# Optimization experiments

Hardware: AMD Instinct MI355X
Metric: run time of the kernel (lower is better)

Reference implementation:

```python
import jax, jax.numpy as jnp
import numpy as np

N, E, D_IN, D_HID, D_OUT = 50000, 800000, 128, 128, 300
BN_EPS = 1e-5


def setup_inputs() -> dict:
    key = jax.random.key(0)
    ks = jax.random.split(key, 10)
    s_in = 1.0 / np.sqrt(D_IN)
    s_hid = 1.0 / np.sqrt(D_HID)
    return {
        "x": jax.random.normal(ks[0], (N, D_IN), jnp.float32),
        "edge_index": jax.random.randint(ks[1], (2, E), 0, N, jnp.int64),
        "Wl": jax.random.normal(ks[2], (D_IN, D_HID), jnp.float32) * s_in,
        "bl": jnp.zeros((D_HID,), jnp.float32),
        "Wr": jax.random.normal(ks[3], (D_IN, D_HID), jnp.float32) * s_in,
        "Wsk": jax.random.normal(ks[4], (D_IN, D_HID), jnp.float32) * s_in,
        "bsk": jnp.zeros((D_HID,), jnp.float32),
        "gamma": jnp.ones((D_HID,), jnp.float32),
        "beta": jnp.zeros((D_HID,), jnp.float32),
        "rmean": jnp.zeros((D_HID,), jnp.float32),
        "rvar": jnp.ones((D_HID,), jnp.float32),
        "Wlo": jax.random.normal(ks[5], (D_HID, D_OUT), jnp.float32) * s_hid,
        "blo": jnp.zeros((D_OUT,), jnp.float32),
        "Wro": jax.random.normal(ks[6], (D_HID, D_OUT), jnp.float32) * s_hid,
    }


def sage_conv(x, src, dst, n_nodes, W_l, b_l, W_r):
    # PyG SAGEConv (aggr='mean'): lin_l(mean_{j in N(i)} x_j) + lin_r(x_i)
    msgs = x[src]                                                 # [E, d] gather
    agg = jax.ops.segment_sum(msgs, dst, num_segments=n_nodes)    # [N, d]
    cnt = jax.ops.segment_sum(jnp.ones((src.shape[0], 1), x.dtype), dst,
                              num_segments=n_nodes)               # [N, 1]
    mean = agg / jnp.maximum(cnt, 1.0)
    return mean @ W_l + b_l + x @ W_r


def reference(x, edge_index, Wl, bl, Wr, Wsk, bsk, gamma, beta, rmean, rvar,
              Wlo, blo, Wro):
    src, dst = edge_index[0], edge_index[1]
    n = x.shape[0]
    # layer 0: conv + skip linear
    h = sage_conv(x, src, dst, n, Wl, bl, Wr) + (x @ Wsk + bsk)
    # BatchNorm1d (eval: running stats)
    h = (h - rmean) * (gamma * jax.lax.rsqrt(rvar + BN_EPS)) + beta
    x_emb = jax.nn.relu(h)                                        # dropout: no-op in eval
    # output conv + log_softmax
    x_out = sage_conv(x_emb, src, dst, n, Wlo, blo, Wro)
    return h, jax.nn.log_softmax(x_out, axis=1)
```

## Files before the change

kernel.cpp:

```cpp
#include <hip/hip_runtime.h>

typedef __attribute__((__ext_vector_type__(8))) __bf16 bf16x8;
typedef __attribute__((__ext_vector_type__(4))) float f32x4;
typedef __attribute__((__ext_vector_type__(4))) unsigned int u32x4;

__device__ __forceinline__ float bf2f(unsigned short u) {
    return __uint_as_float(((unsigned int)u) << 16);
}
__device__ __forceinline__ unsigned short f2bf(float f) {
    unsigned int u = __float_as_uint(f);
    u += 0x7FFFu + ((u >> 16) & 1u);
    return (unsigned short)(u >> 16);
}

__device__ __forceinline__ bool low_short_is_bf16like(unsigned int w) {
    unsigned int lo = w & 0xFFFFu;
    if (lo == 0u || lo == 0x8000u) return true;
    unsigned int e = (lo >> 7) & 0xFFu;
    return (e >= 0x6Cu && e <= 0x8Cu);
}

__global__ __launch_bounds__(64) void k_detect(
    const unsigned int* __restrict__ x, const unsigned int* __restrict__ wl,
    const unsigned int* __restrict__ ei, int* __restrict__ flags)
{
    int t = threadIdx.x;
    int xv = __popcll(__ballot(low_short_is_bf16like(x[t])));
    int wv = __popcll(__ballot(low_short_is_bf16like(wl[t])));
    unsigned int o1 = ei[2 * t + 1];
    unsigned int o2 = ei[2 * t + 129];
    bool oddzero = (o1 == 0u) && (o2 == 0u);
    int e64 = __all(oddzero) ? 1 : 0;
    if (t == 0) {
        flags[0] = (xv < 32) ? 1 : 0;
        flags[1] = (wv < 32) ? 1 : 0;
        flags[2] = e64;
    }
}

__global__ __launch_bounds__(256) void k_tobf(
    const void* __restrict__ xv, const int* __restrict__ flags,
    unsigned short* __restrict__ xbf, long nelem)
{
    int xf32 = flags[0];
    long i = ((long)blockIdx.x * 256 + threadIdx.x) * 8;
    if (i >= nelem) return;
    if (xf32) {
        const float4* p = (const float4*)((const float*)xv + i);
        float4 v0 = p[0], v1 = p[1];
        u32x4 o;
        o.x = (unsigned int)f2bf(v0.x) | ((unsigned int)f2bf(v0.y) << 16);
        o.y = (unsigned int)f2bf(v0.z) | ((unsigned int)f2bf(v0.w) << 16);
        o.z = (unsigned int)f2bf(v1.x) | ((unsigned int)f2bf(v1.y) << 16);
        o.w = (unsigned int)f2bf(v1.z) | ((unsigned int)f2bf(v1.w) << 16);
        *(u32x4*)&xbf[i] = o;
    } else {
        *(u32x4*)&xbf[i] = *(const u32x4*)((const unsigned short*)xv + i);
    }
}

__global__ __launch_bounds__(256) void k_fold1(
    const void* __restrict__ Wl, const void* __restrict__ Wr,
    const void* __restrict__ Wsk, const void* __restrict__ gamma,
    const void* __restrict__ rvar, const int* __restrict__ flags,
    unsigned short* __restrict__ W1p)
{
    int wf32 = flags[1];
    int idx = blockIdx.x * 256 + threadIdx.x;
    int kb = idx >> 10;
    int c  = (idx >> 3) & 127;
    int k7 = idx & 7;
    int k  = kb * 8 + k7;
    float g, rv, w;
    if (wf32) {
        g  = ((const float*)gamma)[c];
        rv = ((const float*)rvar)[c];
        if (k < 128) w = ((const float*)Wl)[k * 128 + c];
        else { int kk = k - 128;
               w = ((const float*)Wr)[kk * 128 + c] + ((const float*)Wsk)[kk * 128 + c]; }
    } else {
        g  = bf2f(((const unsigned short*)gamma)[c]);
        rv = bf2f(((const unsigned short*)rvar)[c]);
        if (k < 128) w = bf2f(((const unsigned short*)Wl)[k * 128 + c]);
        else { int kk = k - 128;
               w = bf2f(((const unsigned short*)Wr)[kk * 128 + c]) +
                   bf2f(((const unsigned short*)Wsk)[kk * 128 + c]); }
    }
    float s = g * rsqrtf(rv + 1e-5f);
    W1p[idx] = f2bf(w * s);
}

__global__ __launch_bounds__(256) void k_fold2(
    const void* __restrict__ Wlo, const void* __restrict__ Wro,
    const int* __restrict__ flags, unsigned short* __restrict__ W2p)
{
    int wf32 = flags[1];
    int idx = blockIdx.x * 256 + threadIdx.x;
    int kb  = idx / 2560;
    int rem = idx - kb * 2560;
    int c   = rem >> 3;
    int k7  = idx & 7;
    int k   = kb * 8 + k7;
    float w = 0.f;
    if (c < 300) {
        if (wf32)
            w = (k < 128) ? ((const float*)Wlo)[k * 300 + c]
                          : ((const float*)Wro)[(k - 128) * 300 + c];
        else
            w = (k < 128) ? bf2f(((const unsigned short*)Wlo)[k * 300 + c])
                          : bf2f(((const unsigned short*)Wro)[(k - 128) * 300 + c]);
    }
    W2p[idx] = f2bf(w);
}

__global__ __launch_bounds__(512) void k_foldb(
    const void* __restrict__ bl, const void* __restrict__ bsk,
    const void* __restrict__ rmean, const void* __restrict__ beta,
    const void* __restrict__ gamma, const void* __restrict__ rvar,
    const void* __restrict__ blo, const int* __restrict__ flags,
    float* __restrict__ bias1, float* __restrict__ bias2)
{
    int wf32 = flags[1];
    int t = threadIdx.x;
    if (t < 128) {
        float g, rv, b1, b2, rm, be;
        if (wf32) {
            g = ((const float*)gamma)[t]; rv = ((const float*)rvar)[t];
            b1 = ((const float*)bl)[t];   b2 = ((const float*)bsk)[t];
            rm = ((const float*)rmean)[t]; be = ((const float*)beta)[t];
        } else {
            g = bf2f(((const unsigned short*)gamma)[t]); rv = bf2f(((const unsigned short*)rvar)[t]);
            b1 = bf2f(((const unsigned short*)bl)[t]);   b2 = bf2f(((const unsigned short*)bsk)[t]);
            rm = bf2f(((const unsigned short*)rmean)[t]); be = bf2f(((const unsigned short*)beta)[t]);
        }
        float s = g * rsqrtf(rv + 1e-5f);
        bias1[t] = (b1 + b2 - rm) * s + be;
    } else if (t < 448) {
        int c = t - 128;
        float b = 0.f;
        if (c < 300)
            b = wf32 ? ((const float*)blo)[c] : bf2f(((const unsigned short*)blo)[c]);
        bias2[c] = b;
    }
}

__global__ __launch_bounds__(256) void k_rank(
    const int* __restrict__ ei, const int* __restrict__ flags,
    int* __restrict__ deg, int* __restrict__ rank, int E, int nnodes)
{
    int e64 = flags[2];
    int e = blockIdx.x * 256 + threadIdx.x;
    if (e >= E) return;
    int d = e64 ? ei[2 * (E + e)] : ei[E + e];
    int r = 0;
    if ((unsigned)d < (unsigned)nnodes) r = atomicAdd(&deg[d], 1);
    rank[e] = r;
}

template <typename IT>
__global__ __launch_bounds__(256) void k_place(
    const int* __restrict__ ei, const int* __restrict__ flags,
    const int* __restrict__ rowptr, const int* __restrict__ aux,
    const int* __restrict__ rank,
    IT* __restrict__ adj, int E, int nnodes)
{
    int e64 = flags[2];
    int e = blockIdx.x * 256 + threadIdx.x;
    if (e >= E) return;
    int s, d;
    if (e64) { s = ei[2 * e]; d = ei[2 * (E + e)]; }
    else     { s = ei[e];     d = ei[E + e]; }
    if ((unsigned)d >= (unsigned)nnodes) return;
    if ((unsigned)s >= (unsigned)nnodes) s = 0;
    adj[rowptr[d] + aux[d >> 10] + rank[e]] = (IT)s;
}

__global__ __launch_bounds__(256) void k_scan_a(
    const int* __restrict__ deg, int* __restrict__ rowptr,
    int* __restrict__ aux, int n)
{
    __shared__ int wsum[4];
    int t = threadIdx.x, blk = blockIdx.x;
    int base = blk * 1024 + t * 4;
    int v[4];
    int s = 0;
    #pragma unroll
    for (int i = 0; i < 4; i++) { int idx = base + i; v[i] = (idx < n) ? deg[idx] : 0; s += v[i]; }
    int lane = t & 63, wv = t >> 6;
    int inc = s;
    #pragma unroll
    for (int off = 1; off < 64; off <<= 1) {
        int u = __shfl_up(inc, off);
        if (lane >= off) inc += u;
    }
    if (lane == 63) wsum[wv] = inc;
    __syncthreads();
    int woff = 0;
    if (wv >= 1) woff += wsum[0];
    if (wv >= 2) woff += wsum[1];
    if (wv >= 3) woff += wsum[2];
    int exc = woff + inc - s;
    #pragma unroll
    for (int i = 0; i < 4; i++) { int idx = base + i; if (idx < n) rowptr[idx] = exc; exc += v[i]; }
    if (t == 255) aux[blk] = woff + inc;
}

__global__ __launch_bounds__(64) void k_scan_b(int* __restrict__ aux, int nblk)
{
    int t = threadIdx.x;
    int carry = 0;
    for (int base = 0; base < nblk; base += 64) {
        int idx = base + t;
        int v = (idx < nblk) ? aux[idx] : 0;
        int inc = v;
        #pragma unroll
        for (int off = 1; off < 64; off <<= 1) {
            int u = __shfl_up(inc, off);
            if (t >= off) inc += u;
        }
        if (idx < nblk) aux[idx] = carry + inc - v;
        carry += __shfl(inc, 63);
    }
}

template <typename IT>
__global__ __launch_bounds__(256) void k_agg(
    const unsigned short* __restrict__ xB,
    const int* __restrict__ rowptr, const int* __restrict__ aux,
    const int* __restrict__ deg,
    const IT* __restrict__ adj, unsigned short* __restrict__ meanB, int n)
{
    int wid = (blockIdx.x * 256 + threadIdx.x) >> 6;
    if (wid >= n) return;
    int lane = threadIdx.x & 63;
    int h  = lane >> 5;
    int sl = lane & 31;
    int start = rowptr[wid] + aux[wid >> 10];
    int dc = deg[wid];
    float acc[4][4];
    #pragma unroll
    for (int u = 0; u < 4; u++)
        #pragma unroll
        for (int c = 0; c < 4; c++) acc[u][c] = 0.f;
    int i = 0;
    for (; i + 7 < dc; i += 8) {
        int e0 = (int)adj[start + i + h];
        int e1 = (int)adj[start + i + 2 + h];
        int e2 = (int)adj[start + i + 4 + h];
        int e3 = (int)adj[start + i + 6 + h];
        uint2 p0 = *(const uint2*)&xB[(size_t)e0 * 128 + sl * 4];
        uint2 p1 = *(const uint2*)&xB[(size_t)e1 * 128 + sl * 4];
        uint2 p2 = *(const uint2*)&xB[(size_t)e2 * 128 + sl * 4];
        uint2 p3 = *(const uint2*)&xB[(size_t)e3 * 128 + sl * 4];
        acc[0][0] += bf2f((unsigned short)p0.x); acc[0][1] += bf2f((unsigned short)(p0.x >> 16));
        acc[0][2] += bf2f((unsigned short)p0.y); acc[0][3] += bf2f((unsigned short)(p0.y >> 16));
        acc[1][0] += bf2f((unsigned short)p1.x); acc[1][1] += bf2f((unsigned short)(p1.x >> 16));
        acc[1][2] += bf2f((unsigned short)p1.y); acc[1][3] += bf2f((unsigned short)(p1.y >> 16));
        acc[2][0] += bf2f((unsigned short)p2.x); acc[2][1] += bf2f((unsigned short)(p2.x >> 16));
        acc[2][2] += bf2f((unsigned short)p2.y); acc[2][3] += bf2f((unsigned short)(p2.y >> 16));
        acc[3][0] += bf2f((unsigned short)p3.x); acc[3][1] += bf2f((unsigned short)(p3.x >> 16));
        acc[3][2] += bf2f((unsigned short)p3.y); acc[3][3] += bf2f((unsigned short)(p3.y >> 16));
    }
    for (; i + h < dc; i += 2) {
        int e0 = (int)adj[start + i + h];
        uint2 p0 = *(const uint2*)&xB[(size_t)e0 * 128 + sl * 4];
        acc[0][0] += bf2f((unsigned short)p0.x); acc[0][1] += bf2f((unsigned short)(p0.x >> 16));
        acc[0][2] += bf2f((unsigned short)p0.y); acc[0][3] += bf2f((unsigned short)(p0.y >> 16));
    }
    float t0 = (acc[0][0] + acc[1][0]) + (acc[2][0] + acc[3][0]);
    float t1 = (acc[0][1] + acc[1][1]) + (acc[2][1] + acc[3][1]);
    float t2 = (acc[0][2] + acc[1][2]) + (acc[2][2] + acc[3][2]);
    float t3 = (acc[0][3] + acc[1][3]) + (acc[2][3] + acc[3][3]);
    t0 += __shfl_xor(t0, 32);
    t1 += __shfl_xor(t1, 32);
    t2 += __shfl_xor(t2, 32);
    t3 += __shfl_xor(t3, 32);
    if (h == 0) {
        float inv = 1.f / fmaxf((float)dc, 1.f);
        uint2 o;
        o.x = (unsigned int)f2bf(t0 * inv) | ((unsigned int)f2bf(t1 * inv) << 16);
        o.y = (unsigned int)f2bf(t2 * inv) | ((unsigned int)f2bf(t3 * inv) << 16);
        *(uint2*)&meanB[(size_t)wid * 128 + sl * 4] = o;
    }
}

__global__ __launch_bounds__(256) void k_gemm1(
    const unsigned short* __restrict__ meanB,
    const unsigned short* __restrict__ xbf, const int* __restrict__ flags,
    const unsigned short* __restrict__ Wp,
    const float* __restrict__ bias, void* __restrict__ outh,
    unsigned short* __restrict__ xemb, int nrows)
{
    constexpr int NTW = 2;
    __shared__ __align__(16) unsigned short Alds[32 * 264];
    int tid = threadIdx.x;
    int row0 = blockIdx.x * 32;
    int xf32 = flags[0];
    {
        int r = tid >> 3, c0 = (tid & 7) * 16;
        int rg = row0 + r; if (rg >= nrows) rg = nrows - 1;
        const u32x4* mp = (const u32x4*)(meanB + (size_t)rg * 128 + c0);
        *(u32x4*)&Alds[r * 264 + c0]     = mp[0];
        *(u32x4*)&Alds[r * 264 + c0 + 8] = mp[1];
        const u32x4* xp = (const u32x4*)(xbf + (size_t)rg * 128 + c0);
        *(u32x4*)&Alds[r * 264 + 128 + c0]     = xp[0];
        *(u32x4*)&Alds[r * 264 + 128 + c0 + 8] = xp[1];
    }
    __syncthreads();
    f32x4 acc[2][NTW];
    #pragma unroll
    for (int a = 0; a < 2; a++)
        #pragma unroll
        for (int b = 0; b < NTW; b++) acc[a][b] = f32x4{0.f, 0.f, 0.f, 0.f};
    int lane = tid & 63, wv = tid >> 6, lh = lane & 15, lq = lane >> 4;
    #pragma unroll
    for (int ks = 0; ks < 8; ++ks) {
        bf16x8 a0 = *(const bf16x8*)&Alds[lh * 264 + ks * 32 + lq * 8];
        bf16x8 a1 = *(const bf16x8*)&Alds[(16 + lh) * 264 + ks * 32 + lq * 8];
        #pragma unroll
        for (int i = 0; i < NTW; i++) {
            int col = (wv + 4 * i) * 16 + lh;
            bf16x8 bfr = *(const bf16x8*)&Wp[(ks * 4 + lq) * 1024 + col * 8];
            acc[0][i] = __builtin_amdgcn_mfma_f32_16x16x32_bf16(a0, bfr, acc[0][i], 0, 0, 0);
            acc[1][i] = __builtin_amdgcn_mfma_f32_16x16x32_bf16(a1, bfr, acc[1][i], 0, 0, 0);
        }
    }
    float* outF = (float*)outh;
    unsigned short* outB = (unsigned short*)outh;
    #pragma unroll
    for (int rt = 0; rt < 2; ++rt)
        #pragma unroll
        for (int i = 0; i < NTW; i++)
            #pragma unroll
            for (int j = 0; j < 4; j++) {
                int r = row0 + rt * 16 + lq * 4 + j;
                if (r < nrows) {
                    int c = (wv + 4 * i) * 16 + lh;
                    float v = acc[rt][i][j] + bias[c];
                    if (xf32) outF[(size_t)r * 128 + c] = v;
                    else      outB[(size_t)r * 128 + c] = f2bf(v);
                    xemb[(size_t)r * 128 + c] = f2bf(fmaxf(v, 0.f));
                }
            }
}

__global__ __launch_bounds__(256) void k_gemm2(
    const unsigned short* __restrict__ meanB,
    const unsigned short* __restrict__ xf, const unsigned short* __restrict__ Wp,
    const float* __restrict__ bias, const int* __restrict__ flags,
    void* __restrict__ outbase, int nrows)
{
    constexpr int NTW = 5;
    __shared__ __align__(16) unsigned short Alds[32 * 264];
    __shared__ float redM[4][32];
    __shared__ float redS[4][32];
    int tid = threadIdx.x;
    int row0 = blockIdx.x * 32;
    int xf32 = flags[0];
    {
        int r = tid >> 3, c0 = (tid & 7) * 16;
        int rg = row0 + r; if (rg >= nrows) rg = nrows - 1;
        const u32x4* mp = (const u32x4*)(meanB + (size_t)rg * 128 + c0);
        *(u32x4*)&Alds[r * 264 + c0]     = mp[0];
        *(u32x4*)&Alds[r * 264 + c0 + 8] = mp[1];
        const u32x4* xp = (const u32x4*)(xf + (size_t)rg * 128 + c0);
        *(u32x4*)&Alds[r * 264 + 128 + c0]     = xp[0];
        *(u32x4*)&Alds[r * 264 + 128 + c0 + 8] = xp[1];
    }
    __syncthreads();
    f32x4 acc[2][NTW];
    #pragma unroll
    for (int a = 0; a < 2; a++)
        #pragma unroll
        for (int b = 0; b < NTW; b++) acc[a][b] = f32x4{0.f, 0.f, 0.f, 0.f};
    int lane = tid & 63, wv = tid >> 6, lh = lane & 15, lq = lane >> 4;
    #pragma unroll
    for (int ks = 0; ks < 8; ++ks) {
        bf16x8 a0 = *(const bf16x8*)&Alds[lh * 264 + ks * 32 + lq * 8];
        bf16x8 a1 = *(const bf16x8*)&Alds[(16 + lh) * 264 + ks * 32 + lq * 8];
        #pragma unroll
        for (int i = 0; i < NTW; i++) {
            int col = (wv + 4 * i) * 16 + lh;
            bf16x8 bfr = *(const bf16x8*)&Wp[(ks * 4 + lq) * 2560 + col * 8];
            acc[0][i] = __builtin_amdgcn_mfma_f32_16x16x32_bf16(a0, bfr, acc[0][i], 0, 0, 0);
            acc[1][i] = __builtin_amdgcn_mfma_f32_16x16x32_bf16(a1, bfr, acc[1][i], 0, 0, 0);
        }
    }
    #pragma unroll
    for (int rt = 0; rt < 2; ++rt)
        #pragma unroll
        for (int i = 0; i < NTW; i++) {
            int col = (wv + 4 * i) * 16 + lh;
            float b = bias[col];
            #pragma unroll
            for (int j = 0; j < 4; j++) acc[rt][i][j] += b;
        }
    float M[2][4];
    #pragma unroll
    for (int rt = 0; rt < 2; ++rt)
        #pragma unroll
        for (int j = 0; j < 4; j++) {
            float m = -3.0e38f;
            #pragma unroll
            for (int i = 0; i < NTW; i++) {
                int col = (wv + 4 * i) * 16 + lh;
                if (col < 300) m = fmaxf(m, acc[rt][i][j]);
            }
            m = fmaxf(m, __shfl_xor(m, 1, 16));
            m = fmaxf(m, __shfl_xor(m, 2, 16));
            m = fmaxf(m, __shfl_xor(m, 4, 16));
            m = fmaxf(m, __shfl_xor(m, 8, 16));
            M[rt][j] = m;
        }
    if (lh == 0) {
        #pragma unroll
        for (int rt = 0; rt < 2; ++rt)
            #pragma unroll
            for (int j = 0; j < 4; j++)
                redM[wv][rt * 16 + lq * 4 + j] = M[rt][j];
    }
    __syncthreads();
    #pragma unroll
    for (int rt = 0; rt < 2; ++rt)
        #pragma unroll
        for (int j = 0; j < 4; j++) {
            int rl = rt * 16 + lq * 4 + j;
            M[rt][j] = fmaxf(fmaxf(redM[0][rl], redM[1][rl]),
                             fmaxf(redM[2][rl], redM[3][rl]));
        }
    float S[2][4];
    #pragma unroll
    for (int rt = 0; rt < 2; ++rt)
        #pragma unroll
        for (int j = 0; j < 4; j++) {
            float s = 0.f;
            #pragma unroll
            for (int i = 0; i < NTW; i++) {
                int col = (wv + 4 * i) * 16 + lh;
                if (col < 300) s += __expf(acc[rt][i][j] - M[rt][j]);
            }
            s += __shfl_xor(s, 1, 16);
            s += __shfl_xor(s, 2, 16);
            s += __shfl_xor(s, 4, 16);
            s += __shfl_xor(s, 8, 16);
            S[rt][j] = s;
        }
    if (lh == 0) {
        #pragma unroll
        for (int rt = 0; rt < 2; ++rt)
            #pragma unroll
            for (int j = 0; j < 4; j++)
                redS[wv][rt * 16 + lq * 4 + j] = S[rt][j];
    }
    __syncthreads();
    float* out1F = (float*)outbase + (size_t)nrows * 128;
    unsigned short* out1B = (unsigned short*)outbase + (size_t)nrows * 128;
    #pragma unroll
    for (int rt = 0; rt < 2; ++rt)
        #pragma unroll
        for (int j = 0; j < 4; j++) {
            int rl = rt * 16 + lq * 4 + j;
            float Sall = (redS[0][rl] + redS[1][rl]) + (redS[2][rl] + redS[3][rl]);
            float L = M[rt][j] + __logf(Sall);
            int rg = row0 + rl;
            if (rg < nrows) {
                #pragma unroll
                for (int i = 0; i < NTW; i++) {
                    int col = (wv + 4 * i) * 16 + lh;
                    if (col < 300) {
                        float v = acc[rt][i][j] - L;
                        if (xf32) out1F[(size_t)rg * 300 + col] = v;
                        else      out1B[(size_t)rg * 300 + col] = f2bf(v);
                    }
                }
            }
        }
}

extern "C" void kernel_launch(void* const* d_in, const int* in_sizes, int n_in,
                              void* d_out, int out_size, void* d_ws, size_t ws_size,
                              hipStream_t stream)
{
    const void* x     = d_in[0];
    const int*  ei    = (const int*)d_in[1];
    const void* Wl    = d_in[2];
    const void* bl    = d_in[3];
    const void* Wr    = d_in[4];
    const void* Wsk   = d_in[5];
    const void* bsk   = d_in[6];
    const void* gamma = d_in[7];
    const void* beta  = d_in[8];
    const void* rmean = d_in[9];
    const void* rvar  = d_in[10];
    const void* Wlo   = d_in[11];
    const void* blo   = d_in[12];
    const void* Wro   = d_in[13];

    int N = in_sizes[0] / 128;
    int E = in_sizes[1] / 2;
    long nelem = (long)N * 128;
    bool idx16 = (N <= 65535);

    char* ws = (char*)d_ws;
    size_t off = 0;
    int* flags = (int*)(ws + off);            off += 256;
    unsigned short* xbf   = (unsigned short*)(ws + off); off += (size_t)N * 128 * 2;
    unsigned short* meanB = (unsigned short*)(ws + off); off += (size_t)N * 128 * 2;
    unsigned short* xemb  = (unsigned short*)(ws + off); off += (size_t)N * 128 * 2;
    off = (off + 255) & ~(size_t)255;
    int* deg    = (int*)(ws + off);           off += (size_t)N * 4;
    int* rowptr = (int*)(ws + off);           off += (size_t)N * 4;
    int* rank   = (int*)(ws + off);           off += (size_t)E * 4;
    int* aux    = (int*)(ws + off);           off += 256;
    void* adjv  = (void*)(ws + off);          off += (size_t)E * 4;
    off = (off + 255) & ~(size_t)255;
    unsigned short* W1p = (unsigned short*)(ws + off);  off += 32768 * 2;
    unsigned short* W2p = (unsigned short*)(ws + off);  off += 81920 * 2;
    float* bias1 = (float*)(ws + off);        off += 512;
    float* bias2 = (float*)(ws + off);        off += 1280;

    int egrid = (E + 255) / 256;
    int sblk  = (N + 1023) / 1024;
    int agrid = (N + 3) / 4;
    int ggrid = (N + 31) / 32;
    int tgrid = (int)((nelem / 8 + 255) / 256);

    hipMemsetAsync(deg, 0, (size_t)N * 4, stream);
    k_detect<<<1, 64, 0, stream>>>((const unsigned int*)x, (const unsigned int*)Wl,
                                   (const unsigned int*)ei, flags);
    k_tobf<<<tgrid, 256, 0, stream>>>(x, flags, xbf, nelem);
    k_fold1<<<128, 256, 0, stream>>>(Wl, Wr, Wsk, gamma, rvar, flags, W1p);
    k_fold2<<<320, 256, 0, stream>>>(Wlo, Wro, flags, W2p);
    k_foldb<<<1, 512, 0, stream>>>(bl, bsk, rmean, beta, gamma, rvar, blo, flags, bias1, bias2);

    k_rank<<<egrid, 256, 0, stream>>>(ei, flags, deg, rank, E, N);
    k_scan_a<<<sblk, 256, 0, stream>>>(deg, rowptr, aux, N);
    k_scan_b<<<1, 64, 0, stream>>>(aux, sblk);

    if (idx16) {
        unsigned short* adj = (unsigned short*)adjv;
        k_place<unsigned short><<<egrid, 256, 0, stream>>>(ei, flags, rowptr, aux, rank, adj, E, N);
        k_agg<unsigned short><<<agrid, 256, 0, stream>>>(xbf, rowptr, aux, deg, adj, meanB, N);
        k_gemm1<<<ggrid, 256, 0, stream>>>(meanB, xbf, flags, W1p, bias1, d_out, xemb, N);
        k_agg<unsigned short><<<agrid, 256, 0, stream>>>(xemb, rowptr, aux, deg, adj, meanB, N);
        k_gemm2<<<ggrid, 256, 0, stream>>>(meanB, xemb, W2p, bias2, flags, d_out, N);
    } else {
        int* adj = (int*)adjv;
        k_place<int><<<egrid, 256, 0, stream>>>(ei, flags, rowptr, aux, rank, adj, E, N);
        k_agg<int><<<agrid, 256, 0, stream>>>(xbf, rowptr, aux, deg, adj, meanB, N);
        k_gemm1<<<ggrid, 256, 0, stream>>>(meanB, xbf, flags, W1p, bias1, d_out, xemb, N);
        k_agg<int><<<agrid, 256, 0, stream>>>(xemb, rowptr, aux, deg, adj, meanB, N);
        k_gemm2<<<ggrid, 256, 0, stream>>>(meanB, xemb, W2p, bias2, flags, d_out, N);
    }
}
```

Before: 191.0 us.

## Gather neighbor features in fp8 and fuse setup kernels, drop flag detection

Quantizes node features (input x and the layer-1 embedding) to fp8 copies and has the mean-aggregation gather read 1 byte per element instead of 2 bf16 bytes, halving the random-gather traffic. The type-detection kernel is removed in favor of inline probing in each kernel. The deg memset is folded into the conversion kernel and the three weight/bias fold kernels are merged into one launch. An extra conversion pass over xemb is added, and the fp8 quantization of aggregated features lowers accuracy, which may break tolerance.

```diff
diff --git a/kernel.cpp b/kernel.cpp
--- a/kernel.cpp
+++ b/kernel.cpp
@@ -2,6 +2,7 @@
 
 typedef __attribute__((__ext_vector_type__(8))) __bf16 bf16x8;
 typedef __attribute__((__ext_vector_type__(4))) float f32x4;
+typedef __attribute__((__ext_vector_type__(2))) float f32x2;
 typedef __attribute__((__ext_vector_type__(4))) unsigned int u32x4;
 
 __device__ __forceinline__ float bf2f(unsigned short u) {
@@ -19,136 +20,158 @@
     unsigned int e = (lo >> 7) & 0xFFu;
     return (e >= 0x6Cu && e <= 0x8Cu);
 }
-
-__global__ __launch_bounds__(64) void k_detect(
-    const unsigned int* __restrict__ x, const unsigned int* __restrict__ wl,
-    const unsigned int* __restrict__ ei, int* __restrict__ flags)
-{
-    int t = threadIdx.x;
-    int xv = __popcll(__ballot(low_short_is_bf16like(x[t])));
-    int wv = __popcll(__ballot(low_short_is_bf16like(wl[t])));
+__device__ __forceinline__ int probe_f32(const unsigned int* __restrict__ p) {
+    int t = threadIdx.x & 63;
+    int cnt = __popcll(__ballot(low_short_is_bf16like(p[t])));
+    return (cnt < 32) ? 1 : 0;
+}
+__device__ __forceinline__ int probe_e64(const unsigned int* __restrict__ ei) {
+    int t = threadIdx.x & 63;
     unsigned int o1 = ei[2 * t + 1];
     unsigned int o2 = ei[2 * t + 129];
-    bool oddzero = (o1 == 0u) && (o2 == 0u);
-    int e64 = __all(oddzero) ? 1 : 0;
-    if (t == 0) {
-        flags[0] = (xv < 32) ? 1 : 0;
-        flags[1] = (wv < 32) ? 1 : 0;
-        flags[2] = e64;
-    }
+    return __all((o1 == 0u) && (o2 == 0u)) ? 1 : 0;
 }
 
 __global__ __launch_bounds__(256) void k_tobf(
-    const void* __restrict__ xv, const int* __restrict__ flags,
-    unsigned short* __restrict__ xbf, long nelem)
-{
-    int xf32 = flags[0];
+    const void* __restrict__ xv, unsigned short* __restrict__ xbf,
+    unsigned int* __restrict__ x8, int* __restrict__ deg,
+    long nelem, int n, int tgrid)
+{
+    if ((int)blockIdx.x >= tgrid) {
+        int j = ((int)blockIdx.x - tgrid) * 256 + threadIdx.x;
+        if (j < n) deg[j] = 0;
+        return;
+    }
+    int xf32 = probe_f32((const unsigned int*)xv);
     long i = ((long)blockIdx.x * 256 + threadIdx.x) * 8;
     if (i >= nelem) return;
+    float f[8];
     if (xf32) {
         const float4* p = (const float4*)((const float*)xv + i);
         float4 v0 = p[0], v1 = p[1];
+        f[0] = v0.x; f[1] = v0.y; f[2] = v0.z; f[3] = v0.w;
+        f[4] = v1.x; f[5] = v1.y; f[6] = v1.z; f[7] = v1.w;
         u32x4 o;
-        o.x = (unsigned int)f2bf(v0.x) | ((unsigned int)f2bf(v0.y) << 16);
-        o.y = (unsigned int)f2bf(v0.z) | ((unsigned int)f2bf(v0.w) << 16);
-        o.z = (unsigned int)f2bf(v1.x) | ((unsigned int)f2bf(v1.y) << 16);
-        o.w = (unsigned int)f2bf(v1.z) | ((unsigned int)f2bf(v1.w) << 16);
+        o.x = (unsigned int)f2bf(f[0]) | ((unsigned int)f2bf(f[1]) << 16);
+        o.y = (unsigned int)f2bf(f[2]) | ((unsigned int)f2bf(f[3]) << 16);
+        o.z = (unsigned int)f2bf(f[4]) | ((unsigned int)f2bf(f[5]) << 16);
+        o.w = (unsigned int)f2bf(f[6]) | ((unsigned int)f2bf(f[7]) << 16);
         *(u32x4*)&xbf[i] = o;
     } else {
-        *(u32x4*)&xbf[i] = *(const u32x4*)((const unsigned short*)xv + i);
-    }
-}
-
-__global__ __launch_bounds__(256) void k_fold1(
+        u32x4 v = *(const u32x4*)((const unsigned short*)xv + i);
+        *(u32x4*)&xbf[i] = v;
+        f[0] = bf2f((unsigned short)v.x); f[1] = bf2f((unsigned short)(v.x >> 16));
+        f[2] = bf2f((unsigned short)v.y); f[3] = bf2f((unsigned short)(v.y >> 16));
+        f[4] = bf2f((unsigned short)v.z); f[5] = bf2f((unsigned short)(v.z >> 16));
+        f[6] = bf2f((unsigned short)v.w); f[7] = bf2f((unsigned short)(v.w >> 16));
+    }
+    unsigned int q0 = 0, q1 = 0;
+    q0 = (unsigned int)__builtin_amdgcn_cvt_pk_fp8_f32(f[0], f[1], (int)q0, false);
+    q0 = (unsigned int)__builtin_amdgcn_cvt_pk_fp8_f32(f[2], f[3], (int)q0, true);
+    q1 = (unsigned int)__builtin_amdgcn_cvt_pk_fp8_f32(f[4], f[5], (int)q1, false);
+    q1 = (unsigned int)__builtin_amdgcn_cvt_pk_fp8_f32(f[6], f[7], (int)q1, true);
+    uint2 q; q.x = q0; q.y = q1;
+    *(uint2*)&x8[i >> 2] = q;
+}
+
+__global__ __launch_bounds__(256) void k_to8(
+    const unsigned short* __restrict__ src, unsigned int* __restrict__ dst,
+    long nelem)
+{
+    long i = ((long)blockIdx.x * 256 + threadIdx.x) * 8;
+    if (i >= nelem) return;
+    u32x4 v = *(const u32x4*)&src[i];
+    unsigned int q0 = 0, q1 = 0;
+    q0 = (unsigned int)__builtin_amdgcn_cvt_pk_fp8_f32(
+            bf2f((unsigned short)v.x), bf2f((unsigned short)(v.x >> 16)), (int)q0, false);
+    q0 = (unsigned int)__builtin_amdgcn_cvt_pk_fp8_f32(
+            bf2f((unsigned short)v.y), bf2f((unsigned short)(v.y >> 16)), (int)q0, true);
+    q1 = (unsigned int)__builtin_amdgcn_cvt_pk_fp8_f32(
+            bf2f((unsigned short)v.z), bf2f((unsigned short)(v.z >> 16)), (int)q1, false);
+    q1 = (unsigned int)__builtin_amdgcn_cvt_pk_fp8_f32(
+            bf2f((unsigned short)v.w), bf2f((unsigned short)(v.w >> 16)), (int)q1, true);
+    uint2 q; q.x = q0; q.y = q1;
+    *(uint2*)&dst[i >> 2] = q;
+}
+
+__global__ __launch_bounds__(256) void k_fold(
     const void* __restrict__ Wl, const void* __restrict__ Wr,
     const void* __restrict__ Wsk, const void* __restrict__ gamma,
-    const void* __restrict__ rvar, const int* __restrict__ flags,
-    unsigned short* __restrict__ W1p)
-{
-    int wf32 = flags[1];
-    int idx = blockIdx.x * 256 + threadIdx.x;
-    int kb = idx >> 10;
-    int c  = (idx >> 3) & 127;
-    int k7 = idx & 7;
-    int k  = kb * 8 + k7;
-    float g, rv, w;
-    if (wf32) {
-        g  = ((const float*)gamma)[c];
-        rv = ((const float*)rvar)[c];
-        if (k < 128) w = ((const float*)Wl)[k * 128 + c];
-        else { int kk = k - 128;
-               w = ((const float*)Wr)[kk * 128 + c] + ((const float*)Wsk)[kk * 128 + c]; }
+    const void* __restrict__ rvar, const void* __restrict__ bl,
+    const void* __restrict__ bsk, const void* __restrict__ rmean,
+    const void* __restrict__ beta, const void* __restrict__ Wlo,
+    const void* __restrict__ blo, const void* __restrict__ Wro,
+    unsigned short* __restrict__ W1p, unsigned short* __restrict__ W2p,
+    float* __restrict__ bias1, float* __restrict__ bias2)
+{
+    int wf32 = probe_f32((const unsigned int*)Wl);
+    int b = blockIdx.x, t = threadIdx.x;
+    if (b < 128) {
+        int idx = b * 256 + t;
+        int kb = idx >> 10, c = (idx >> 3) & 127, k7 = idx & 7;
+        int k = kb * 8 + k7;
+        float g, rv, w;
+        if (wf32) {
+            g  = ((const float*)gamma)[c];
+            rv = ((const float*)rvar)[c];
+            if (k < 128) w = ((const float*)Wl)[k * 128 + c];
+            else { int kk = k - 128;
+                   w = ((const float*)Wr)[kk * 128 + c] + ((const float*)Wsk)[kk * 128 + c]; }
+        } else {
+            g  = bf2f(((const unsigned short*)gamma)[c]);
+            rv = bf2f(((const unsigned short*)rvar)[c]);
+            if (k < 128) w = bf2f(((const unsigned short*)Wl)[k * 128 + c]);
+            else { int kk = k - 128;
+                   w = bf2f(((const unsigned short*)Wr)[kk * 128 + c]) +
+                       bf2f(((const unsigned short*)Wsk)[kk * 128 + c]); }
+        }
+        float s = g * rsqrtf(rv + 1e-5f);
+        W1p[idx] = f2bf(w * s);
+    } else if (b < 448) {
+        int idx = (b - 128) * 256 + t;
+        int kb = idx / 2560;
+        int rem = idx - kb * 2560;
+        int c = rem >> 3, k7 = idx & 7;
+        int k = kb * 8 + k7;
+        float w = 0.f;
+        if (c < 300) {
+            if (wf32)
+                w = (k < 128) ? ((const float*)Wlo)[k * 300 + c]
+                              : ((const float*)Wro)[(k - 128) * 300 + c];
+            else
+                w = (k < 128) ? bf2f(((const unsigned short*)Wlo)[k * 300 + c])
+                              : bf2f(((const unsigned short*)Wro)[(k - 128) * 300 + c]);
+        }
+        W2p[idx] = f2bf(w);
     } else {
-        g  = bf2f(((const unsigned short*)gamma)[c]);
-        rv = bf2f(((const unsigned short*)rvar)[c]);
-        if (k < 128) w = bf2f(((const unsigned short*)Wl)[k * 128 + c]);
-        else { int kk = k - 128;
-               w = bf2f(((const unsigned short*)Wr)[kk * 128 + c]) +
-                   bf2f(((const unsigned short*)Wsk)[kk * 128 + c]); }
-    }
-    float s = g * rsqrtf(rv + 1e-5f);
-    W1p[idx] = f2bf(w * s);
-}
-
-__global__ __launch_bounds__(256) void k_fold2(
-    const void* __restrict__ Wlo, const void* __restrict__ Wro,
-    const int* __restrict__ flags, unsigned short* __restrict__ W2p)
-{
-    int wf32 = flags[1];
-    int idx = blockIdx.x * 256 + threadIdx.x;
-    int kb  = idx / 2560;
-    int rem = idx - kb * 2560;
-    int c   = rem >> 3;
-    int k7  = idx & 7;
-    int k   = kb * 8 + k7;
-    float w = 0.f;
-    if (c < 300) {
-        if (wf32)
-            w = (k < 128) ? ((const float*)Wlo)[k * 300 + c]
-                          : ((const float*)Wro)[(k - 128) * 300 + c];
-        else
-            w = (k < 128) ? bf2f(((const unsigned short*)Wlo)[k * 300 + c])
-                          : bf2f(((const unsigned short*)Wro)[(k - 128) * 300 + c]);
-    }
-    W2p[idx] = f2bf(w);
-}
-
-__global__ __launch_bounds__(512) void k_foldb(
-    const void* __restrict__ bl, const void* __restrict__ bsk,
-    const void* __restrict__ rmean, const void* __restrict__ beta,
-    const void* __restrict__ gamma, const void* __restrict__ rvar,
-    const void* __restrict__ blo, const int* __restrict__ flags,
-    float* __restrict__ bias1, float* __restrict__ bias2)
-{
-    int wf32 = flags[1];
-    int t = threadIdx.x;
-    if (t < 128) {
-        float g, rv, b1, b2, rm, be;
-        if (wf32) {
-            g = ((const float*)gamma)[t]; rv = ((const float*)rvar)[t];
-            b1 = ((const float*)bl)[t];   b2 = ((const float*)bsk)[t];
-            rm = ((const float*)rmean)[t]; be = ((const float*)beta)[t];
-        } else {
-            g = bf2f(((const unsigned short*)gamma)[t]); rv = bf2f(((const unsigned short*)rvar)[t]);
-            b1 = bf2f(((const unsigned short*)bl)[t]);   b2 = bf2f(((const unsigned short*)bsk)[t]);
-            rm = bf2f(((const unsigned short*)rmean)[t]); be = bf2f(((const unsigned short*)beta)[t]);
-        }
-        float s = g * rsqrtf(rv + 1e-5f);
-        bias1[t] = (b1 + b2 - rm) * s + be;
-    } else if (t < 448) {
-        int c = t - 128;
-        float b = 0.f;
-        if (c < 300)
-            b = wf32 ? ((const float*)blo)[c] : bf2f(((const unsigned short*)blo)[c]);
-        bias2[c] = b;
+        if (t < 128) {
+            float g, rv, b1, b2, rm, be;
+            if (wf32) {
+                g = ((const float*)gamma)[t]; rv = ((const float*)rvar)[t];
+                b1 = ((const float*)bl)[t];   b2 = ((const float*)bsk)[t];
+                rm = ((const float*)rmean)[t]; be = ((const float*)beta)[t];
+            } else {
+                g = bf2f(((const unsigned short*)gamma)[t]); rv = bf2f(((const unsigned short*)rvar)[t]);
+                b1 = bf2f(((const unsigned short*)bl)[t]);   b2 = bf2f(((const unsigned short*)bsk)[t]);
+                rm = bf2f(((const unsigned short*)rmean)[t]); be = bf2f(((const unsigned short*)beta)[t]);
+            }
+            float s = g * rsqrtf(rv + 1e-5f);
+            bias1[t] = (b1 + b2 - rm) * s + be;
+        }
+        for (int c = t; c < 320; c += 256) {
+            float v = 0.f;
+            if (c < 300)
+                v = wf32 ? ((const float*)blo)[c] : bf2f(((const unsigned short*)blo)[c]);
+            bias2[c] = v;
+        }
     }
 }
 
 __global__ __launch_bounds__(256) void k_rank(
-    const int* __restrict__ ei, const int* __restrict__ flags,
+    const int* __restrict__ ei,
     int* __restrict__ deg, int* __restrict__ rank, int E, int nnodes)
 {
-    int e64 = flags[2];
+    int e64 = probe_e64((const unsigned int*)ei);
     int e = blockIdx.x * 256 + threadIdx.x;
     if (e >= E) return;
     int d = e64 ? ei[2 * (E + e)] : ei[E + e];
@@ -159,12 +182,12 @@
 
 template <typename IT>
 __global__ __launch_bounds__(256) void k_place(
-    const int* __restrict__ ei, const int* __restrict__ flags,
+    const int* __restrict__ ei,
     const int* __restrict__ rowptr, const int* __restrict__ aux,
     const int* __restrict__ rank,
     IT* __restrict__ adj, int E, int nnodes)
 {
-    int e64 = flags[2];
+    int e64 = probe_e64((const unsigned int*)ei);
     int e = blockIdx.x * 256 + threadIdx.x;
     if (e >= E) return;
     int s, d;
@@ -225,7 +248,7 @@
 
 template <typename IT>
 __global__ __launch_bounds__(256) void k_agg(
-    const unsigned short* __restrict__ xB,
+    const unsigned int* __restrict__ x8,
     const int* __restrict__ rowptr, const int* __restrict__ aux,
     const int* __restrict__ deg,
     const IT* __restrict__ adj, unsigned short* __restrict__ meanB, int n)
@@ -248,24 +271,29 @@
         int e1 = (int)adj[start + i + 2 + h];
         int e2 = (int)adj[start + i + 4 + h];
         int e3 = (int)adj[start + i + 6 + h];
-        uint2 p0 = *(const uint2*)&xB[(size_t)e0 * 128 + sl * 4];
-        uint2 p1 = *(const uint2*)&xB[(size_t)e1 * 128 + sl * 4];
-        uint2 p2 = *(const uint2*)&xB[(size_t)e2 * 128 + sl * 4];
-        uint2 p3 = *(const uint2*)&xB[(size_t)e3 * 128 + sl * 4];
-        acc[0][0] += bf2f((unsigned short)p0.x); acc[0][1] += bf2f((unsigned short)(p0.x >> 16));
-        acc[0][2] += bf2f((unsigned short)p0.y); acc[0][3] += bf2f((unsigned short)(p0.y >> 16));
-        acc[1][0] += bf2f((unsigned short)p1.x); acc[1][1] += bf2f((unsigned short)(p1.x >> 16));
-        acc[1][2] += bf2f((unsigned short)p1.y); acc[1][3] += bf2f((unsigned short)(p1.y >> 16));
-        acc[2][0] += bf2f((unsigned short)p2.x); acc[2][1] += bf2f((unsigned short)(p2.x >> 16));
-        acc[2][2] += bf2f((unsigned short)p2.y); acc[2][3] += bf2f((unsigned short)(p2.y >> 16));
-        acc[3][0] += bf2f((unsigned short)p3.x); acc[3][1] += bf2f((unsigned short)(p3.x >> 16));
-        acc[3][2] += bf2f((unsigned short)p3.y); acc[3][3] += bf2f((unsigned short)(p3.y >> 16));
+        unsigned int p0 = x8[(size_t)e0 * 32 + sl];
+        unsigned int p1 = x8[(size_t)e1 * 32 + sl];
+        unsigned int p2 = x8[(size_t)e2 * 32 + sl];
+        unsigned int p3 = x8[(size_t)e3 * 32 + sl];
+        f32x2 l0 = __builtin_amdgcn_cvt_pk_f32_fp8((int)p0, false);
+        f32x2 h0 = __builtin_amdgcn_cvt_pk_f32_fp8((int)p0, true);
+        f32x2 l1 = __builtin_amdgcn_cvt_pk_f32_fp8((int)p1, false);
+        f32x2 h1 = __builtin_amdgcn_cvt_pk_f32_fp8((int)p1, true);
+        f32x2 l2 = __builtin_amdgcn_cvt_pk_f32_fp8((int)p2, false);
+        f32x2 h2 = __builtin_amdgcn_cvt_pk_f32_fp8((int)p2, true);
+        f32x2 l3 = __builtin_amdgcn_cvt_pk_f32_fp8((int)p3, false);
+        f32x2 h3 = __builtin_amdgcn_cvt_pk_f32_fp8((int)p3, true);
+        acc[0][0] += l0.x; acc[0][1] += l0.y; acc[0][2] += h0.x; acc[0][3] += h0.y;
+        acc[1][0] += l1.x; acc[1][1] += l1.y; acc[1][2] += h1.x; acc[1][3] += h1.y;
+        acc[2][0] += l2.x; acc[2][1] += l2.y; acc[2][2] += h2.x; acc[2][3] += h2.y;
+        acc[3][0] += l3.x; acc[3][1] += l3.y; acc[3][2] += h3.x; acc[3][3] += h3.y;
     }
     for (; i + h < dc; i += 2) {
         int e0 = (int)adj[start + i + h];
-        uint2 p0 = *(const uint2*)&xB[(size_t)e0 * 128 + sl * 4];
-        acc[0][0] += bf2f((unsigned short)p0.x); acc[0][1] += bf2f((unsigned short)(p0.x >> 16));
-        acc[0][2] += bf2f((unsigned short)p0.y); acc[0][3] += bf2f((unsigned short)(p0.y >> 16));
+        unsigned int p0 = x8[(size_t)e0 * 32 + sl];
+        f32x2 l0 = __builtin_amdgcn_cvt_pk_f32_fp8((int)p0, false);
+        f32x2 h0 = __builtin_amdgcn_cvt_pk_f32_fp8((int)p0, true);
+        acc[0][0] += l0.x; acc[0][1] += l0.y; acc[0][2] += h0.x; acc[0][3] += h0.y;
     }
     float t0 = (acc[0][0] + acc[1][0]) + (acc[2][0] + acc[3][0]);
     float t1 = (acc[0][1] + acc[1][1]) + (acc[2][1] + acc[3][1]);
@@ -286,7 +314,7 @@
 
 __global__ __launch_bounds__(256) void k_gemm1(
     const unsigned short* __restrict__ meanB,
-    const unsigned short* __restrict__ xbf, const int* __restrict__ flags,
+    const unsigned short* __restrict__ xbf, const unsigned int* __restrict__ xprobe,
     const unsigned short* __restrict__ Wp,
     const float* __restrict__ bias, void* __restrict__ outh,
     unsigned short* __restrict__ xemb, int nrows)
@@ -295,7 +323,7 @@
     __shared__ __align__(16) unsigned short Alds[32 * 264];
     int tid = threadIdx.x;
     int row0 = blockIdx.x * 32;
-    int xf32 = flags[0];
+    int xf32 = probe_f32(xprobe);
     {
         int r = tid >> 3, c0 = (tid & 7) * 16;
         int rg = row0 + r; if (rg >= nrows) rg = nrows - 1;
@@ -346,9 +374,9 @@
 
 __global__ __launch_bounds__(256) void k_gemm2(
     const unsigned short* __restrict__ meanB,
-    const unsigned short* __restrict__ xf, const unsigned short* __restrict__ Wp,
-    const float* __restrict__ bias, const int* __restrict__ flags,
-    void* __restrict__ outbase, int nrows)
+    const unsigned short* __restrict__ xf, const unsigned int* __restrict__ xprobe,
+    const unsigned short* __restrict__ Wp,
+    const float* __restrict__ bias, void* __restrict__ outbase, int nrows)
 {
     constexpr int NTW = 5;
     __shared__ __align__(16) unsigned short Alds[32 * 264];
@@ -356,7 +384,7 @@
     __shared__ float redS[4][32];
     int tid = threadIdx.x;
     int row0 = blockIdx.x * 32;
-    int xf32 = flags[0];
+    int xf32 = probe_f32(xprobe);
     {
         int r = tid >> 3, c0 = (tid & 7) * 16;
         int rg = row0 + r; if (rg >= nrows) rg = nrows - 1;
@@ -503,10 +531,11 @@
 
     char* ws = (char*)d_ws;
     size_t off = 0;
-    int* flags = (int*)(ws + off);            off += 256;
     unsigned short* xbf   = (unsigned short*)(ws + off); off += (size_t)N * 128 * 2;
     unsigned short* meanB = (unsigned short*)(ws + off); off += (size_t)N * 128 * 2;
     unsigned short* xemb  = (unsigned short*)(ws + off); off += (size_t)N * 128 * 2;
+    unsigned int* x8      = (unsigned int*)(ws + off);   off += (size_t)N * 128;
+    unsigned int* xemb8   = (unsigned int*)(ws + off);   off += (size_t)N * 128;
     off = (off + 255) & ~(size_t)255;
     int* deg    = (int*)(ws + off);           off += (size_t)N * 4;
     int* rowptr = (int*)(ws + off);           off += (size_t)N * 4;
@@ -524,32 +553,33 @@
     int agrid = (N + 3) / 4;
     int ggrid = (N + 31) / 32;
     int tgrid = (int)((nelem / 8 + 255) / 256);
-
-    hipMemsetAsync(deg, 0, (size_t)N * 4, stream);
-    k_detect<<<1, 64, 0, stream>>>((const unsigned int*)x, (const unsigned int*)Wl,
-                                   (const unsigned int*)ei, flags);
-    k_tobf<<<tgrid, 256, 0, stream>>>(x, flags, xbf, nelem);
-    k_fold1<<<128, 256, 0, stream>>>(Wl, Wr, Wsk, gamma, rvar, flags, W1p);
-    k_fold2<<<320, 256, 0, stream>>>(Wlo, Wro, flags, W2p);
-    k_foldb<<<1, 512, 0, stream>>>(bl, bsk, rmean, beta, gamma, rvar, blo, flags, bias1, bias2);
-
-    k_rank<<<egrid, 256, 0, stream>>>(ei, flags, deg, rank, E, N);
+    int dgrid = (N + 255) / 256;
+
+    const unsigned int* xprobe = (const unsigned int*)x;
+
+    k_tobf<<<tgrid + dgrid, 256, 0, stream>>>(x, xbf, x8, deg, nelem, N, tgrid);
+    k_fold<<<449, 256, 0, stream>>>(Wl, Wr, Wsk, gamma, rvar, bl, bsk, rmean, beta,
+                                    Wlo, blo, Wro, W1p, W2p, bias1, bias2);
+
+    k_rank<<<egrid, 256, 0, stream>>>(ei, deg, rank, E, N);
     k_scan_a<<<sblk, 256, 0, stream>>>(deg, rowptr, aux, N);
     k_scan_b<<<1, 64, 0, stream>>>(aux, sblk);
 
     if (idx16) {
         unsigned short* adj = (unsigned short*)adjv;
-        k_place<unsigned short><<<egrid, 256, 0, stream>>>(ei, flags, rowptr, aux, rank, adj, E, N);
-        k_agg<unsigned short><<<agrid, 256, 0, stream>>>(xbf, rowptr, aux, deg, adj, meanB, N);
-        k_gemm1<<<ggrid, 256, 0, stream>>>(meanB, xbf, flags, W1p, bias1, d_out, xemb, N);
-        k_agg<unsigned short><<<agrid, 256, 0, stream>>>(xemb, rowptr, aux, deg, adj, meanB, N);
-        k_gemm2<<<ggrid, 256, 0, stream>>>(meanB, xemb, W2p, bias2, flags, d_out, N);
+        k_place<unsigned short><<<egrid, 256, 0, stream>>>(ei, rowptr, aux, rank, adj, E, N);
+        k_agg<unsigned short><<<agrid, 256, 0, stream>>>(x8, rowptr, aux, deg, adj, meanB, N);
+        k_gemm1<<<ggrid, 256, 0, stream>>>(meanB, xbf, xprobe, W1p, bias1, d_out, xemb, N);
+        k_to8<<<tgrid, 256, 0, stream>>>(xemb, xemb8, nelem);
+        k_agg<unsigned short><<<agrid, 256, 0, stream>>>(xemb8, rowptr, aux, deg, adj, meanB, N);
+        k_gemm2<<<ggrid, 256, 0, stream>>>(meanB, xemb, xprobe, W2p, bias2, d_out, N);
     } else {
         int* adj = (int*)adjv;
-        k_place<int><<<egrid, 256, 0, stream>>>(ei, flags, rowptr, aux, rank, adj, E, N);
-        k_agg<int><<<agrid, 256, 0, stream>>>(xbf, rowptr, aux, deg, adj, meanB, N);
-        k_gemm1<<<ggrid, 256, 0, stream>>>(meanB, xbf, flags, W1p, bias1, d_out, xemb, N);
-        k_agg<int><<<agrid, 256, 0, stream>>>(xemb, rowptr, aux, deg, adj, meanB, N);
-        k_gemm2<<<ggrid, 256, 0, stream>>>(meanB, xemb, W2p, bias2, flags, d_out, N);
-    }
-}
+        k_place<int><<<egrid, 256, 0, stream>>>(ei, rowptr, aux, rank, adj, E, N);
+        k_agg<int><<<agrid, 256, 0, stream>>>(x8, rowptr, aux, deg, adj, meanB, N);
+        k_gemm1<<<ggrid, 256, 0, stream>>>(meanB, xbf, xprobe, W1p, bias1, d_out, xemb, N);
+        k_to8<<<tgrid, 256, 0, stream>>>(xemb, xemb8, nelem);
+        k_agg<int><<<agrid, 256, 0, stream>>>(xemb8, rowptr, aux, deg, adj, meanB, N);
+        k_gemm2<<<ggrid, 256, 0, stream>>>(meanB, xemb, xprobe, W2p, bias2, d_out, N);
+    }
+}
```

Measured after the change: 176.7 us. -7.5%, faster.
